# Kernel tuning notes

Measured on AMD Instinct MI355X. Metric: run time of the kernel, lower is better.

## Reference

```python
import jax, jax.numpy as jnp
import numpy as np
from jax import lax

EPS = 1e-10
ALPHA = 1000.0

def _gauss_kernel(k=3, mu=0.0, sigma=3.0):
    g1 = np.linspace(-1.0, 1.0, k)
    x, y = np.meshgrid(g1, g1)
    d = np.sqrt(x ** 2 + y ** 2)
    g = np.exp(-(d - mu) ** 2 / (2.0 * sigma ** 2)) / (2.0 * np.pi * sigma ** 2)
    return jnp.asarray(g / g.sum(), jnp.float32)

def _sobel_kernel(k=3, transpose=False):
    r = np.linspace(-(k // 2), k // 2, k)
    x, y = np.meshgrid(r, r)
    den = x ** 2 + y ** 2
    den[:, k // 2] = 1.0
    s = x / den
    if transpose:
        s = s.T
    return jnp.asarray(s, jnp.float32)

def _canny_nms_kernels():
    # 8 directional difference kernels (center minus neighbor), E, SE, S, SW, W, NW, N, NE
    off = [(1, 2), (2, 2), (2, 1), (2, 0), (1, 0), (0, 0), (0, 1), (0, 2)]
    k = np.zeros((8, 3, 3), np.float32)
    k[:, 1, 1] = 1.0
    for i, (r, c) in enumerate(off):
        k[i, r, c] = -1.0
    return jnp.asarray(k)

def _dwconv_reflect(x, k2d):
    # depthwise 3x3 conv with reflect padding (same as padding_mode='reflect', groups=C)
    C = x.shape[1]
    xp = jnp.pad(x, ((0, 0), (0, 0), (1, 1), (1, 1)), mode='reflect')
    w = jnp.broadcast_to(k2d[None, None], (C, 1, 3, 3))
    return lax.conv_general_dilated(xp, w, (1, 1), 'VALID', feature_group_count=C)

def _forward(x, w_expand, w_perm_gauss, w_perm_sx, w_perm_sy, w_merge, low_t, high_t):
    gauss = _gauss_kernel(3, 0.0, 3.0)
    sob_x = _sobel_kernel(3, transpose=False)
    sob_y = _sobel_kernel(3, transpose=True)
    canny = _canny_nms_kernels()  # (8,3,3)
    # 1x1 channel expansion
    h = jnp.einsum('oc,bchw->bohw', w_expand, x)
    # gaussian blur (depthwise) + trainable 1x1 permute
    g = jnp.einsum('oc,bchw->bohw', w_perm_gauss, _dwconv_reflect(h, gauss))
    gx = jnp.einsum('oc,bchw->bohw', w_perm_sx, _dwconv_reflect(g, sob_x))
    gy = jnp.einsum('oc,bchw->bohw', w_perm_sy, _dwconv_reflect(g, sob_y))
    mag = jnp.sqrt(gx * gx + gy * gy + EPS)  # (B,C,H,W)
    # NMSConv2d: every output kernel applies the same directional diff summed over ALL input
    # channels, so the 8C outputs repeat with period 8 -> compute 8 dirs on the channel-sum.
    s = jnp.sum(mag, axis=1, keepdims=True)  # (B,1,H,W)
    dirs = lax.conv_general_dilated(s, canny[:, None], (1, 1), [(1, 1), (1, 1)])  # (B,8,H,W)
    deg = jnp.arctan2(gy, gx) * (180.0 / np.pi)
    idx = jnp.mod(jnp.round(deg / 45.0), 8.0).astype(jnp.int32)  # (B,C,H,W) in [0,8)
    pos = jnp.take_along_axis(dirs[:, None], idx[:, :, None], axis=2)[:, :, 0]
    neg = jnp.take_along_axis(dirs[:, None], ((idx + 4) % 8)[:, :, None], axis=2)[:, :, 0]
    nms = mag * ((pos > 0) & (neg > 0)).astype(mag.dtype)
    # soft double threshold (steep sigmoids)
    strong = jax.nn.sigmoid(ALPHA * (nms - high_t))
    weak = 0.5 * (jax.nn.sigmoid(ALPHA * (high_t - nms)) - jax.nn.sigmoid(ALPHA * (low_t - nms)))
    thr = weak + strong
    # merge C -> 1
    m = jnp.einsum('oc,bchw->bohw', w_merge, thr)  # (B,1,H,W)
    # one-step hysteresis: strong pixels promote neighbouring weak (==0.5) pixels
    img_strong = jnp.where(m == 1.0, m, 0.0)
    masked = (m == 0.5)
    hyst = _dwconv_reflect(img_strong, jnp.full((3, 3), 1.25, m.dtype))
    changed = jnp.where((hyst > 1.0) & masked, m, 0.0) + img_strong
    return changed

def setup_inputs() -> dict:
    key = jax.random.key(0)
    k0, k1, k2 = jax.random.split(key, 3)
    B, Cin, C, H, W = 8, 3, 8, 512, 512
    x = jax.random.uniform(k0, (B, Cin, H, W), jnp.float32)
    w_expand = jax.nn.softmax(jax.random.uniform(k1, (C, Cin), jnp.float32), axis=0)
    eye = jnp.eye(C, dtype=jnp.float32)
    bound = 1.0 / np.sqrt(C)
    w_merge = jax.random.uniform(k2, (1, C), jnp.float32, minval=-bound, maxval=bound)
    low_t = jnp.full((C, 1, 1), 0.1, jnp.float32)
    high_t = jnp.full((C, 1, 1), 0.2, jnp.float32)
    return {'x': x, 'w_expand': w_expand, 'w_perm_gauss': eye, 'w_perm_sx': eye,
            'w_perm_sy': eye, 'w_merge': w_merge, 'low_t': low_t, 'high_t': high_t}

def reference(x, w_expand, w_perm_gauss, w_perm_sx, w_perm_sy, w_merge, low_t, high_t):
    return _forward(x, w_expand, w_perm_gauss, w_perm_sx, w_perm_sy, w_merge, low_t, high_t)
```

## Files before the change

kernel.cpp:

```cpp
#include <hip/hip_runtime.h>
#include <math.h>

#define Bsz 8
#define HWp (512*512)
#define TS 32
#define SG 36
#define MG 34
#define XW 40
#define BW 38
#define NT 512
#define K2E 1442.6950408889634f
#define T2q 0.17157287525380993f

#if __has_builtin(__builtin_amdgcn_exp2f)
#define EXP2F(x) __builtin_amdgcn_exp2f(x)
#else
#define EXP2F(x) __expf(0.6931471805599453f*(x))
#endif

__device__ __forceinline__ int refl(int i, int n) {
    i = (i < 0) ? -i : i;
    return (i >= n) ? (2*n - 2 - i) : i;
}

__global__ void k_mats(const float* __restrict__ we, const float* __restrict__ pg,
                       const float* __restrict__ psx, const float* __restrict__ psy,
                       const float* __restrict__ wm, const float* __restrict__ lowt,
                       const float* __restrict__ hight, float* __restrict__ mats) {
    if (threadIdx.x == 0 && blockIdx.x == 0) {
        float M1[8][3];
        for (int o = 0; o < 8; ++o)
            for (int c = 0; c < 3; ++c) {
                float a = 0.f;
                for (int k = 0; k < 8; ++k) a += pg[o*8+k] * we[k*3+c];
                M1[o][c] = a;
            }
        for (int o = 0; o < 8; ++o)
            for (int c = 0; c < 3; ++c) {
                float a = 0.f, b = 0.f;
                for (int k = 0; k < 8; ++k) { a += psx[o*8+k]*M1[k][c]; b += psy[o*8+k]*M1[k][c]; }
                mats[o*3+c]      = a;
                mats[24 + o*3+c] = b;
            }
        for (int o = 0; o < 8; ++o) {
            mats[48+o] = hight[o] * K2E;
            mats[56+o] = lowt[o]  * K2E;
            mats[64+o] = 0.5f * wm[o];
        }
    }
}

__global__ __launch_bounds__(NT) void k_fused(
    const float* __restrict__ x, const float* __restrict__ mats,
    float* __restrict__ out, float wc, float wE, float wk)
{
    __shared__ float sm1[3*XW*XW];
    __shared__ float blb[3*BW*BW];
    __shared__ int anyS;

    const int b  = blockIdx.z;
    const int x0 = blockIdx.x*TS, y0 = blockIdx.y*TS;
    const int t  = threadIdx.x;
    const bool inter = (blockIdx.x > 0) && ((int)blockIdx.x < (int)gridDim.x-1) &&
                       (blockIdx.y > 0) && ((int)blockIdx.y < (int)gridDim.y-1);

    if (t == 0) anyS = 0;

    const float* xb = x + (size_t)b*3*HWp;

    if (inter) {
        const float* xo = xb + (size_t)(y0-4)*512 + (x0-4);
        for (int i = t; i < 3*XW*10; i += NT) {
            int c = i/400; int j = i - c*400; int r = j/10; int q = j - r*10;
            float4 v = *(const float4*)(xo + (size_t)c*HWp + r*512 + q*4);
            *(float4*)&sm1[c*(XW*XW) + r*XW + q*4] = v;
        }
    } else {
        for (int i = t; i < XW*XW; i += NT) {
            int r = i/XW, cc = i - r*XW;
            size_t off = (size_t)refl(y0-4+r,512)*512 + refl(x0-4+cc,512);
            #pragma unroll
            for (int c = 0; c < 3; ++c)
                sm1[c*(XW*XW)+i] = xb[(size_t)c*HWp + off];
        }
    }
    __syncthreads();

    if (inter) {
        if (t < 494) {
            int g = t/38, cb = t - g*38, r0 = 3*g;
            #pragma unroll
            for (int c = 0; c < 3; ++c) {
                const float* col = &sm1[c*(XW*XW) + cb];
                float* bo = &blb[c*(BW*BW) + cb];
                float a0 = col[r0*XW],     a1 = col[r0*XW+1],     a2 = col[r0*XW+2];
                float e0 = col[(r0+1)*XW], e1 = col[(r0+1)*XW+1], e2 = col[(r0+1)*XW+2];
                #pragma unroll
                for (int ir = 0; ir < 3; ++ir) {
                    int r = r0 + ir;
                    if (r < BW) {
                        float f0 = col[(r+2)*XW], f1 = col[(r+2)*XW+1], f2 = col[(r+2)*XW+2];
                        float t0 = a0+f0, t1 = a1+f1, t2 = a2+f2;
                        float u = t0+t2, v = e0+e2, w = t1+v;
                        bo[r*BW] = wk*u + wE*w + wc*e1;
                        a0=e0; a1=e1; a2=e2; e0=f0; e1=f1; e2=f2;
                    }
                }
            }
        }
    } else {
        for (int i = t; i < BW*BW; i += NT) {
            int r = i/BW, cc = i - r*BW;
            int iy = refl(y0-3+r,512) - (y0-4);
            int ix = refl(x0-3+cc,512) - (x0-4);
            const int base = iy*XW + ix;
            #pragma unroll
            for (int c = 0; c < 3; ++c) {
                const float* xp = &sm1[c*(XW*XW) + base];
                blb[c*(BW*BW)+i] =
                    wk*(xp[-XW-1]+xp[-XW+1]+xp[XW-1]+xp[XW+1]) +
                    wE*(xp[-XW]+xp[-1]+xp[1]+xp[XW]) + wc*xp[0];
            }
        }
    }
    __syncthreads();

    float mg[3][8];
    unsigned qk[3];
    const int gC = t/36, csC = t - gC*36, r0C = 3*gC;
    const bool actC = (t < 432);
    if (actC) {
        float txv[3][3], tyv[3][3];
        #pragma unroll
        for (int c = 0; c < 3; ++c) {
            const float* blc = &blb[c*(BW*BW) + csC];
            float p0 = blc[r0C*BW],     p1 = blc[r0C*BW+1],     p2 = blc[r0C*BW+2];
            float q0 = blc[(r0C+1)*BW], q1 = blc[(r0C+1)*BW+1], q2 = blc[(r0C+1)*BW+2];
            float D0 = p2-p0, E0 = fmaf(0.5f, p0+p2, p1);
            float D1 = q2-q0, E1 = fmaf(0.5f, q0+q2, q1);
            #pragma unroll
            for (int ir = 0; ir < 3; ++ir) {
                const float* wr = &blc[(r0C+2+ir)*BW];
                float w0 = wr[0], w1 = wr[1], w2 = wr[2];
                float D2 = w2-w0, E2 = fmaf(0.5f, w0+w2, w1);
                txv[ir][c] = fmaf(0.5f, D0+D2, D1);
                tyv[ir][c] = E2 - E0;
                D0 = D1; D1 = D2; E0 = E1; E1 = E2;
            }
        }
        #pragma unroll
        for (int ir = 0; ir < 3; ++ir) {
            float s = 0.f; unsigned pk = 0;
            #pragma unroll
            for (int o = 0; o < 8; ++o) {
                float gx = mats[o*3]*txv[ir][0]    + mats[o*3+1]*txv[ir][1]    + mats[o*3+2]*txv[ir][2];
                float gy = mats[24+o*3]*tyv[ir][0] + mats[24+o*3+1]*tyv[ir][1] + mats[24+o*3+2]*tyv[ir][2];
                float gx2 = gx*gx, gy2 = gy*gy;
                float mag = __builtin_amdgcn_sqrtf(gx2 + gy2 + 1e-10f);
                mg[ir][o] = mag; s += mag;
                unsigned dv = 1u | (((__float_as_uint(gx) ^ __float_as_uint(gy)) >> 30) & 2u);
                unsigned qo = (gx2 <= T2q*gy2) ? 2u : dv;
                qo = (gy2 <= T2q*gx2) ? 0u : qo;
                pk |= qo << (2*o);
            }
            qk[ir] = pk;
            #pragma unroll
            for (int o = 0; o < 8; ++o) { asm volatile("" : "+v"(mg[ir][o])); }
            asm volatile("" : "+v"(qk[ir]));
            int rr = r0C + ir;
            int gy_ = y0-2+rr, gx_ = x0-2+csC;
            bool inimg = ((unsigned)gy_ < 512u) && ((unsigned)gx_ < 512u);
            sm1[rr*SG + csC] = inimg ? s : 0.f;
        }
    }
    __syncthreads();

    {
        const float* sS = sm1;
        float* mS = sm1 + SG*SG;
        const float* hiK = mats + 48;
        const float* loK = mats + 56;
        const float* wmh = mats + 64;
        if (actC && csC >= 1 && csC <= 34) {
            #pragma unroll
            for (int ir = 0; ir < 3; ++ir) {
                int r = r0C + ir;
                if (r >= 1 && r <= 34) {
                    const float* sp = &sS[r*SG + csC];
                    float sc = sp[0];
                    unsigned mask = 0;
                    mask |= ((sc > sp[1])    && (sc > sp[-1]))    ? 1u : 0u;
                    mask |= ((sc > sp[SG+1]) && (sc > sp[-SG-1])) ? 2u : 0u;
                    mask |= ((sc > sp[SG])   && (sc > sp[-SG]))   ? 4u : 0u;
                    mask |= ((sc > sp[SG-1]) && (sc > sp[-SG+1])) ? 8u : 0u;
                    unsigned pk = qk[ir];
                    float m = 0.f;
                    #pragma unroll
                    for (int o = 0; o < 8; ++o) {
                        float nms = ((mask >> ((pk >> (2*o)) & 3u)) & 1u) ? mg[ir][o] : 0.f;
                        float shi = __builtin_amdgcn_rcpf(1.f + EXP2F(fmaf(nms, -K2E, hiK[o])));
                        float slo = __builtin_amdgcn_rcpf(1.f + EXP2F(fmaf(nms, -K2E, loK[o])));
                        m += wmh[o]*(shi + slo);
                    }
                    mS[(r-1)*MG + (csC-1)] = m;
                    if (m == 1.0f) anyS = 1;
                }
            }
        }
    }
    __syncthreads();

    {
        const float* mS = sm1 + SG*SG;
        float* op = out + (size_t)b*HWp;
        if (anyS == 0) {
            #pragma unroll
            for (int i2 = t; i2 < TS*TS; i2 += NT) {
                int ty_ = i2>>5, tx_ = i2&31;
                op[(size_t)(y0+ty_)*512 + (x0+tx_)] = 0.f;
            }
        } else {
            for (int i2 = t; i2 < TS*TS; i2 += NT) {
                int ty_ = i2>>5, tx_ = i2&31;
                int y = y0 + ty_, xg = x0 + tx_;
                const float* mp = &mS[(ty_+1)*MG + (tx_+1)];
                float mc = mp[0];
                float hy = 0.f;
                if (inter) {
                    #pragma unroll
                    for (int dy = -1; dy <= 1; ++dy)
                        #pragma unroll
                        for (int dx = -1; dx <= 1; ++dx)
                            hy += (mp[dy*MG+dx] == 1.0f) ? 1.25f : 0.f;
                } else {
                    #pragma unroll
                    for (int dy = -1; dy <= 1; ++dy)
                        #pragma unroll
                        for (int dx = -1; dx <= 1; ++dx) {
                            int ly = refl(y+dy,512) - (y0-1);
                            int lx = refl(xg+dx,512) - (x0-1);
                            hy += (mS[ly*MG+lx] == 1.0f) ? 1.25f : 0.f;
                        }
                }
                float strong = (mc == 1.0f) ? mc : 0.f;
                op[(size_t)y*512 + xg] =
                    (((hy > 1.0f) && (mc == 0.5f)) ? mc : 0.f) + strong;
            }
        }
    }
}

extern "C" void kernel_launch(void* const* d_in, const int* in_sizes, int n_in,
                              void* d_out, int out_size, void* d_ws, size_t ws_size,
                              hipStream_t stream) {
    const float* x    = (const float*)d_in[0];
    const float* we   = (const float*)d_in[1];
    const float* pg   = (const float*)d_in[2];
    const float* psx  = (const float*)d_in[3];
    const float* psy  = (const float*)d_in[4];
    const float* wm   = (const float*)d_in[5];
    const float* lowt = (const float*)d_in[6];
    const float* hit  = (const float*)d_in[7];
    float* mats = (float*)d_ws;
    float* outp = (float*)d_out;

    double e1 = exp(-1.0/18.0), e2 = exp(-2.0/18.0);
    double sum = 1.0 + 4.0*e1 + 4.0*e2;
    float wc = (float)(1.0/sum), wE = (float)(e1/sum), wk = (float)(e2/sum);

    k_mats<<<1, 64, 0, stream>>>(we, pg, psx, psy, wm, lowt, hit, mats);
    k_fused<<<dim3(512/TS, 512/TS, Bsz), dim3(NT), 0, stream>>>(
        x, mats, outp, wc, wE, wk);
}
```

Baseline: 52.43 us.

## Pack magnitude/sigmoid math into float2 vectors, slide NMS window, vectorize zero stores

Precomputes interleaved gradient weight matrices so the gradient and threshold sigmoid math works on float2 pairs, letting the compiler use packed FP32 instructions. The NMS stage now slides a 3x3 register window down rows instead of reloading all neighbours from LDS for each row. The strong-pixel flag is collected per thread and written to shared memory once, and all-zero tiles are stored with float4 writes. These changes add register pressure and rely on the compiler actually emitting packed ops.

New measurement: 52.17 us. About the same (-0.5%).

```diff
diff --git a/kernel.cpp b/kernel.cpp
--- a/kernel.cpp
+++ b/kernel.cpp
@@ -11,6 +11,8 @@
 #define NT 512
 #define K2E 1442.6950408889634f
 #define T2q 0.17157287525380993f
+
+typedef float f2 __attribute__((ext_vector_type(2)));
 
 #if __has_builtin(__builtin_amdgcn_exp2f)
 #define EXP2F(x) __builtin_amdgcn_exp2f(x)
@@ -47,6 +49,12 @@
             mats[56+o] = lowt[o]  * K2E;
             mats[64+o] = 0.5f * wm[o];
         }
+        for (int j = 0; j < 4; ++j)
+            for (int k = 0; k < 3; ++k)
+                for (int e = 0; e < 2; ++e) {
+                    mats[72  + (j*3+k)*2 + e] = mats[(2*j+e)*3 + k];
+                    mats[120 + (j*3+k)*2 + e] = mats[24 + (2*j+e)*3 + k];
+                }
     }
 }
 
@@ -99,11 +107,11 @@
                 for (int ir = 0; ir < 3; ++ir) {
                     int r = r0 + ir;
                     if (r < BW) {
-                        float f0 = col[(r+2)*XW], f1 = col[(r+2)*XW+1], f2 = col[(r+2)*XW+2];
-                        float t0 = a0+f0, t1 = a1+f1, t2 = a2+f2;
+                        float f0 = col[(r+2)*XW], f1 = col[(r+2)*XW+1], f2v = col[(r+2)*XW+2];
+                        float t0 = a0+f0, t1 = a1+f1, t2 = a2+f2v;
                         float u = t0+t2, v = e0+e2, w = t1+v;
                         bo[r*BW] = wk*u + wE*w + wc*e1;
-                        a0=e0; a1=e1; a2=e2; e0=f0; e1=f1; e2=f2;
+                        a0=e0; a1=e1; a2=e2; e0=f0; e1=f1; e2=f2v;
                     }
                 }
             }
@@ -148,20 +156,29 @@
                 D0 = D1; D1 = D2; E0 = E1; E1 = E2;
             }
         }
+        const f2* A2 = (const f2*)(mats + 72);
+        const f2* B2 = (const f2*)(mats + 120);
         #pragma unroll
         for (int ir = 0; ir < 3; ++ir) {
-            float s = 0.f; unsigned pk = 0;
-            #pragma unroll
-            for (int o = 0; o < 8; ++o) {
-                float gx = mats[o*3]*txv[ir][0]    + mats[o*3+1]*txv[ir][1]    + mats[o*3+2]*txv[ir][2];
-                float gy = mats[24+o*3]*tyv[ir][0] + mats[24+o*3+1]*tyv[ir][1] + mats[24+o*3+2]*tyv[ir][2];
-                float gx2 = gx*gx, gy2 = gy*gy;
-                float mag = __builtin_amdgcn_sqrtf(gx2 + gy2 + 1e-10f);
-                mg[ir][o] = mag; s += mag;
-                unsigned dv = 1u | (((__float_as_uint(gx) ^ __float_as_uint(gy)) >> 30) & 2u);
-                unsigned qo = (gx2 <= T2q*gy2) ? 2u : dv;
-                qo = (gy2 <= T2q*gx2) ? 0u : qo;
-                pk |= qo << (2*o);
+            f2 s2 = {0.f, 0.f};
+            unsigned pk = 0;
+            #pragma unroll
+            for (int j = 0; j < 4; ++j) {
+                f2 gx = A2[j*3+0]*txv[ir][0] + A2[j*3+1]*txv[ir][1] + A2[j*3+2]*txv[ir][2];
+                f2 gy = B2[j*3+0]*tyv[ir][0] + B2[j*3+1]*tyv[ir][1] + B2[j*3+2]*tyv[ir][2];
+                f2 gx2 = gx*gx, gy2 = gy*gy;
+                f2 r2 = gx2 + gy2 + (f2){1e-10f, 1e-10f};
+                float m0 = __builtin_amdgcn_sqrtf(r2.x);
+                float m1 = __builtin_amdgcn_sqrtf(r2.y);
+                mg[ir][2*j] = m0; mg[ir][2*j+1] = m1;
+                s2 += (f2){m0, m1};
+                unsigned d0 = 1u | (((__float_as_uint(gx.x) ^ __float_as_uint(gy.x)) >> 30) & 2u);
+                unsigned q0 = (gx2.x <= T2q*gy2.x) ? 2u : d0;
+                q0 = (gy2.x <= T2q*gx2.x) ? 0u : q0;
+                unsigned d1 = 1u | (((__float_as_uint(gx.y) ^ __float_as_uint(gy.y)) >> 30) & 2u);
+                unsigned q1 = (gx2.y <= T2q*gy2.y) ? 2u : d1;
+                q1 = (gy2.y <= T2q*gx2.y) ? 0u : q1;
+                pk |= (q0 << (4*j)) | (q1 << (4*j+2));
             }
             qk[ir] = pk;
             #pragma unroll
@@ -170,54 +187,79 @@
             int rr = r0C + ir;
             int gy_ = y0-2+rr, gx_ = x0-2+csC;
             bool inimg = ((unsigned)gy_ < 512u) && ((unsigned)gx_ < 512u);
-            sm1[rr*SG + csC] = inimg ? s : 0.f;
+            sm1[rr*SG + csC] = inimg ? (s2.x + s2.y) : 0.f;
         }
     }
     __syncthreads();
 
+    bool anyL = false;
     {
         const float* sS = sm1;
         float* mS = sm1 + SG*SG;
-        const float* hiK = mats + 48;
-        const float* loK = mats + 56;
-        const float* wmh = mats + 64;
+        const f2* hiK2 = (const f2*)(mats + 48);
+        const f2* loK2 = (const f2*)(mats + 56);
+        const f2* wm2  = (const f2*)(mats + 64);
         if (actC && csC >= 1 && csC <= 34) {
+            int ra = r0C-1 < 0 ? 0 : r0C-1;
+            int rb = r0C;
+            int rc = r0C+1;
+            const float* pa = &sS[ra*SG + csC];
+            const float* pb = &sS[rb*SG + csC];
+            const float* pc = &sS[rc*SG + csC];
+            float l0=pa[-1], c0=pa[0], r0v=pa[1];
+            float l1=pb[-1], c1=pb[0], r1v=pb[1];
+            float l2=pc[-1], c2=pc[0], r2v=pc[1];
             #pragma unroll
             for (int ir = 0; ir < 3; ++ir) {
                 int r = r0C + ir;
                 if (r >= 1 && r <= 34) {
-                    const float* sp = &sS[r*SG + csC];
-                    float sc = sp[0];
+                    float sc = c1;
                     unsigned mask = 0;
-                    mask |= ((sc > sp[1])    && (sc > sp[-1]))    ? 1u : 0u;
-                    mask |= ((sc > sp[SG+1]) && (sc > sp[-SG-1])) ? 2u : 0u;
-                    mask |= ((sc > sp[SG])   && (sc > sp[-SG]))   ? 4u : 0u;
-                    mask |= ((sc > sp[SG-1]) && (sc > sp[-SG+1])) ? 8u : 0u;
+                    mask |= ((sc > r1v) && (sc > l1)) ? 1u : 0u;
+                    mask |= ((sc > r2v) && (sc > l0)) ? 2u : 0u;
+                    mask |= ((sc > c2)  && (sc > c0)) ? 4u : 0u;
+                    mask |= ((sc > l2)  && (sc > r0v)) ? 8u : 0u;
                     unsigned pk = qk[ir];
-                    float m = 0.f;
+                    f2 acc = {0.f, 0.f};
                     #pragma unroll
-                    for (int o = 0; o < 8; ++o) {
-                        float nms = ((mask >> ((pk >> (2*o)) & 3u)) & 1u) ? mg[ir][o] : 0.f;
-                        float shi = __builtin_amdgcn_rcpf(1.f + EXP2F(fmaf(nms, -K2E, hiK[o])));
-                        float slo = __builtin_amdgcn_rcpf(1.f + EXP2F(fmaf(nms, -K2E, loK[o])));
-                        m += wmh[o]*(shi + slo);
+                    for (int j = 0; j < 4; ++j) {
+                        unsigned ii = pk >> (4*j);
+                        f2 nms;
+                        nms.x = ((mask >> (ii & 3u)) & 1u)      ? mg[ir][2*j]   : 0.f;
+                        nms.y = ((mask >> ((ii>>2) & 3u)) & 1u) ? mg[ir][2*j+1] : 0.f;
+                        f2 aH = nms * (f2){-K2E,-K2E} + hiK2[j];
+                        f2 aL = nms * (f2){-K2E,-K2E} + loK2[j];
+                        f2 sh = { __builtin_amdgcn_rcpf(1.f + EXP2F(aH.x)),
+                                  __builtin_amdgcn_rcpf(1.f + EXP2F(aH.y)) };
+                        f2 sl = { __builtin_amdgcn_rcpf(1.f + EXP2F(aL.x)),
+                                  __builtin_amdgcn_rcpf(1.f + EXP2F(aL.y)) };
+                        acc += wm2[j]*(sh + sl);
                     }
+                    float m = acc.x + acc.y;
                     mS[(r-1)*MG + (csC-1)] = m;
-                    if (m == 1.0f) anyS = 1;
-                }
-            }
-        }
-    }
+                    anyL |= (m == 1.0f);
+                }
+                if (ir < 2) {
+                    int rn = r0C + 2 + ir; rn = rn > 35 ? 35 : rn;
+                    const float* pn = &sS[rn*SG + csC];
+                    l0=l1; c0=c1; r0v=r1v;
+                    l1=l2; c1=c2; r1v=r2v;
+                    l2=pn[-1]; c2=pn[0]; r2v=pn[1];
+                }
+            }
+        }
+    }
+    if (anyL) anyS = 1;
     __syncthreads();
 
     {
         const float* mS = sm1 + SG*SG;
         float* op = out + (size_t)b*HWp;
         if (anyS == 0) {
-            #pragma unroll
-            for (int i2 = t; i2 < TS*TS; i2 += NT) {
-                int ty_ = i2>>5, tx_ = i2&31;
-                op[(size_t)(y0+ty_)*512 + (x0+tx_)] = 0.f;
+            if (t < 256) {
+                int row = t >> 3, q = t & 7;
+                float4 z = {0.f, 0.f, 0.f, 0.f};
+                *(float4*)(op + (size_t)(y0+row)*512 + x0 + q*4) = z;
             }
         } else {
             for (int i2 = t; i2 < TS*TS; i2 += NT) {
```
